# Kernel tuning notes

Measured on AMD Instinct MI355X. Metric: run time of the kernel, lower is better.

The kernel has to match this reference:

```python
import jax, jax.numpy as jnp
import numpy as np

LMAX = 5
RESOLUTION = 12
ASPECT_RATIO = 2
BATCH = 256
NB = 2 * RESOLUTION                       # res_beta = 24
NA = round(2 * ASPECT_RATIO * RESOLUTION)  # res_alpha = res_gamma = 48
DIM = sum((2 * l + 1) ** 2 for l in range(LMAX + 1))  # 286

# normalize2mom constant for tanh: (E_{z~N(0,1)}[tanh(z)^2])^{-1/2}
_x = np.linspace(-12.0, 12.0, 1_000_001)
_pdf = np.exp(-0.5 * _x * _x) / np.sqrt(2.0 * np.pi)
ACT_CST = float(np.trapz(np.tanh(_x) ** 2 * _pdf, _x) ** -0.5)  # ~1.5927


def _su2_generators(j):
    m = np.arange(-j, j)
    raising = np.diag(-np.sqrt(j * (j + 1) - m * (m + 1)), k=-1).astype(complex)
    m = np.arange(-j + 1, j + 1)
    lowering = np.diag(np.sqrt(j * (j + 1) - m * (m - 1)), k=1).astype(complex)
    m = np.arange(-j, j + 1)
    return np.stack([0.5 * (raising + lowering), np.diag(1j * m), -0.5j * (raising - lowering)])


def _q_real_to_complex(l):
    q = np.zeros((2 * l + 1, 2 * l + 1), dtype=complex)
    for m in range(-l, 0):
        q[l + m, l + abs(m)] = 1 / np.sqrt(2)
        q[l + m, l - abs(m)] = -1j / np.sqrt(2)
    q[l, l] = 1
    for m in range(1, l + 1):
        q[l + m, l + abs(m)] = (-1) ** m / np.sqrt(2)
        q[l + m, l - abs(m)] = 1j * (-1) ** m / np.sqrt(2)
    return (-1j) ** l * q


def _so3_generators(l):
    X = _su2_generators(l)
    Q = _q_real_to_complex(l)
    return np.real(np.conj(Q.T)[None] @ X @ Q[None])  # real [3, 2l+1, 2l+1]


def _expm_angles(A, t):
    """exp(t_n * A) for real antisymmetric A via eigendecomposition. -> [n, d, d] real"""
    vals, vecs = np.linalg.eig(A.astype(complex))
    inv = np.linalg.inv(vecs)
    phases = np.exp(t[:, None] * vals[None, :])  # [n, d]
    return np.real(np.einsum('ij,nj,jk->nik', vecs, phases, inv))


def _build_D_and_qw():
    # Euler angle grids (e3nn SO3Grid convention)
    b = (np.arange(NB) + 0.5) / NB * np.pi          # beta   [nb]
    a = np.arange(NA) / NA * 2.0 * np.pi            # alpha=gamma [na]
    blocks = []
    for l in range(LMAX + 1):
        X = _so3_generators(l)
        Ra = _expm_angles(X[1], a)   # exp(alpha * X1)  [na,d,d]
        Rb = _expm_angles(X[0], b)   # exp(beta  * X0)  [nb,d,d]
        # D^l(a,b,c) = Ra[a] @ Rb[b] @ Ra[c]
        Dl = np.einsum('xij,yjk,zkl->xyzil', Ra, Rb, Ra)
        blocks.append(np.sqrt(2 * l + 1) * Dl.reshape(NA, NB, NA, -1))
    D = np.concatenate(blocks, axis=-1).astype(np.float32)  # [na, nb, na, dim]
    # lie_learn / Kostelec-Rockmore quadrature weights for beta
    bb = NB // 2
    k = np.arange(bb)
    j = np.arange(2 * bb)
    w = (2.0 / bb) * np.sin(np.pi * (2 * j + 1) / (4.0 * bb)) * np.sum(
        (1.0 / (2 * k + 1))[None, :]
        * np.sin((2 * j[:, None] + 1) * (2 * k[None, :] + 1) * np.pi / (4.0 * bb)),
        axis=1,
    )
    w = w / (2.0 * (2 * bb) ** 2)
    qw = (w * NB ** 2 / NA ** 2).astype(np.float32)  # [nb]
    return jnp.asarray(D), jnp.asarray(qw)


def setup_inputs() -> dict:
    key = jax.random.key(0)
    features = jax.random.normal(key, (BATCH, DIM), dtype=jnp.float32)
    D, qw = _build_D_and_qw()
    return {"features": features, "D": D, "qw": qw}


def reference(features, D, qw):
    dim = D.shape[-1]
    s = jnp.sqrt(jnp.asarray(dim, features.dtype))
    # to_grid: [B, dim] x [na, nb, na, dim] -> [B, na, nb, na]
    g = jnp.einsum('bi,xyzi->bxyz', features, D) / s
    # normalized pointwise nonlinearity on SO(3) samples
    g = ACT_CST * jnp.tanh(g)
    # from_grid: quadrature-weighted projection back onto flat Wigner basis
    return jnp.einsum('bxyz,y,xyzi->bi', g, qw, D) * s
```

## Files before the change

### kernel.cpp

```cpp
#include <hip/hip_runtime.h>
#include <hip/hip_bf16.h>

#define DIM    286
#define DIMP   288
#define NZTOT  55296
#define NBATCH 256
#define NB_    24
#define NA_    48
#define ZC     32
#define NTILES 1728
#define NCHUNK 192
#define TILES_PER_WG 9
#define S_CONST 16.911534525287763f
#define INV_S   0.05913123959890826f
#define ACT_CST 1.5927f

typedef short bf16x8 __attribute__((ext_vector_type(8)));
typedef float f32x4  __attribute__((ext_vector_type(4)));

#define WS_FBF  0u
#define WS_DBF  147456u
#define WS_DT   (WS_DBF + 31850496u)
#define WS_PART (WS_DT + 31850496u)

typedef const __attribute__((address_space(1))) char GA;
typedef __attribute__((address_space(3))) char LA;
__device__ __forceinline__ void gload_lds16(const void* g, void* l) {
    __builtin_amdgcn_global_load_lds((GA*)g, (LA*)l, 16, 0, 0);
}

__global__ void k_prep(const float* __restrict__ F, const float* __restrict__ D,
                       const float* __restrict__ qw,
                       __hip_bfloat16* __restrict__ Fbf,
                       __hip_bfloat16* __restrict__ Dbf, __hip_bfloat16* __restrict__ Dt2) {
    __shared__ float T[32][305];
    __shared__ float qs[24];
    int t = threadIdx.x;
    int bid = blockIdx.x;
    if (bid >= NTILES) {
        int o = (bid - NTILES) * 256 + t;
        int row = o / DIMP, col = o % DIMP;
        float v = (col < DIM) ? F[row * DIM + col] * INV_S : 0.f;
        Fbf[o] = __float2bfloat16(v);
        return;
    }
    int z0 = bid * 32;
    if (t < 24) qs[t] = qw[t] * S_CONST;
    const float4* Df = (const float4*)(D + (size_t)z0 * DIM);
    for (int k = 0; k < 9; ++k) {
        int idx = t + k * 256;
        if (idx < 2288) {
            float4 v = Df[idx];
            int e = idx * 4;
            int z = e / DIM, i = e % DIM;
            __hip_bfloat162 lo, hi;
            lo.x = __float2bfloat16(v.x); lo.y = __float2bfloat16(v.y);
            hi.x = __float2bfloat16(v.z); hi.y = __float2bfloat16(v.w);
            T[z][i] = v.x; T[z][i + 1] = v.y;
            *(__hip_bfloat162*)(Dbf + (size_t)(z0 + z) * DIMP + i) = lo;
            if (i == 284) {
                T[z + 1][0] = v.z; T[z + 1][1] = v.w;
                *(__hip_bfloat162*)(Dbf + (size_t)(z0 + z + 1) * DIMP) = hi;
            } else {
                T[z][i + 2] = v.z; T[z][i + 3] = v.w;
                *(__hip_bfloat162*)(Dbf + (size_t)(z0 + z) * DIMP + i + 2) = hi;
            }
        }
    }
    if (t < 32) {
        __hip_bfloat162 zz; zz.x = __float2bfloat16(0.f); zz.y = zz.x;
        *(__hip_bfloat162*)(Dbf + (size_t)(z0 + t) * DIMP + DIM) = zz;
    }
    __syncthreads();
    for (int s = 0; s < 5; ++s) {
        int idx = t + s * 256;
        if (idx < 1152) {
            int i = idx >> 2, zc = idx & 3;
            __hip_bfloat16 o8[8];
            #pragma unroll
            for (int j = 0; j < 8; ++j) {
                int zl = zc * 8 + j;
                int y = ((z0 + zl) / NA_) % NB_;
                o8[j] = __float2bfloat16(T[zl][i] * qs[y]);
            }
            *(bf16x8*)(Dt2 + ((size_t)bid * DIMP + i) * ZC + zc * 8) = *(const bf16x8*)o8;
        }
    }
}

__launch_bounds__(256, 2)
__global__ void k_main(const __hip_bfloat16* __restrict__ Fbf,
                       const __hip_bfloat16* __restrict__ Dbf,
                       const __hip_bfloat16* __restrict__ Dt2,
                       float* __restrict__ part) {
    __shared__ __align__(16) __hip_bfloat16 Ds[2][32][288];
    __shared__ __align__(16) __hip_bfloat16 Dts[2][288][32];
    __shared__ __align__(16) __hip_bfloat16 Gs[4][16][40];

    int t = threadIdx.x;
    int wave = t >> 6, lane = t & 63, ln = lane & 15, q = lane >> 4;

    bf16x8 fa[9];
    int row = blockIdx.y * 64 + wave * 16 + ln;
    const __hip_bfloat16* fp = Fbf + (size_t)row * DIMP + q * 8;
    #pragma unroll
    for (int ks = 0; ks < 9; ++ks) fa[ks] = *(const bf16x8*)(fp + ks * 32);

    f32x4 acc[18];
    #pragma unroll
    for (int n = 0; n < 18; ++n) acc[n] = (f32x4){0.f, 0.f, 0.f, 0.f};

    auto stage = [&](int tz, int b) {
        const char* src; char* dst;
        if (wave < 2) {
            src = (const char*)(Dbf + (size_t)tz * ZC * DIMP) + wave * 9216 + lane * 16;
            dst = ((char*)&Ds[b][0][0]) + wave * 9216;
        } else {
            src = (const char*)(Dt2 + (size_t)tz * DIMP * ZC) + (wave - 2) * 9216 + lane * 16;
            dst = ((char*)&Dts[b][0][0]) + (wave - 2) * 9216;
        }
        #pragma unroll
        for (int j = 0; j < 9; ++j)
            gload_lds16(src + j * 1024, dst + j * 1024);
    };

    stage(blockIdx.x, 0);

    #pragma unroll 1
    for (int k = 0; k < TILES_PER_WG; ++k) {
        asm volatile("s_waitcnt vmcnt(0)" ::: "memory");
        __syncthreads();
        if (k + 1 < TILES_PER_WG) stage(blockIdx.x + (k + 1) * NCHUNK, (k + 1) & 1);
        int b = k & 1;
        f32x4 g0 = (f32x4){0.f,0.f,0.f,0.f}, g1 = (f32x4){0.f,0.f,0.f,0.f};
        #pragma unroll
        for (int ks = 0; ks < 9; ++ks) {
            bf16x8 b0 = *(const bf16x8*)(&Ds[b][ln][ks * 32 + q * 8]);
            bf16x8 b1 = *(const bf16x8*)(&Ds[b][16 + ln][ks * 32 + q * 8]);
            g0 = __builtin_amdgcn_mfma_f32_16x16x32_bf16(fa[ks], b0, g0, 0, 0, 0);
            g1 = __builtin_amdgcn_mfma_f32_16x16x32_bf16(fa[ks], b1, g1, 0, 0, 0);
        }
        #pragma unroll
        for (int nf = 0; nf < 2; ++nf) {
            #pragma unroll
            for (int r = 0; r < 4; ++r) {
                float x = (nf == 0) ? g0[r] : g1[r];
                float a = fabsf(x);
                float e = __expf(-2.f * a);
                float th = (1.f - e) / (1.f + e);
                float v = copysignf(ACT_CST * th, x);
                Gs[wave][q * 4 + r][nf * 16 + ln] = __float2bfloat16(v);
            }
        }
        bf16x8 a2 = *(const bf16x8*)(&Gs[wave][ln][q * 8]);
        #pragma unroll
        for (int nf = 0; nf < 18; ++nf) {
            bf16x8 b2 = *(const bf16x8*)(&Dts[b][nf * 16 + ln][q * 8]);
            acc[nf] = __builtin_amdgcn_mfma_f32_16x16x32_bf16(a2, b2, acc[nf], 0, 0, 0);
        }
    }
    float* pb = part + ((size_t)blockIdx.x * NBATCH + blockIdx.y * 64 + wave * 16) * DIMP;
    #pragma unroll
    for (int nf = 0; nf < 18; ++nf) {
        #pragma unroll
        for (int r = 0; r < 4; ++r) {
            pb[(size_t)(q * 4 + r) * DIMP + nf * 16 + ln] = acc[nf][r];
        }
    }
}

__global__ void k_reduce(const float* __restrict__ part, float* __restrict__ out) {
    __shared__ float4 red[3][16];
    int t = threadIdx.x, wave = t >> 6, lane = t & 63;
    int j = lane & 15;
    int zg = wave * 4 + (lane >> 4);
    int o4 = blockIdx.x * 16 + j;
    int b = o4 / 72, c4 = o4 % 72;
    const float* p = part + (size_t)b * DIMP + c4 * 4;
    float4 s = make_float4(0.f, 0.f, 0.f, 0.f);
    #pragma unroll 4
    for (int ii = 0; ii < 12; ++ii) {
        float4 v = *(const float4*)(p + (size_t)(zg * 12 + ii) * NBATCH * DIMP);
        s.x += v.x; s.y += v.y; s.z += v.z; s.w += v.w;
    }
    s.x += __shfl_down(s.x, 16); s.y += __shfl_down(s.y, 16);
    s.z += __shfl_down(s.z, 16); s.w += __shfl_down(s.w, 16);
    s.x += __shfl_down(s.x, 32); s.y += __shfl_down(s.y, 32);
    s.z += __shfl_down(s.z, 32); s.w += __shfl_down(s.w, 32);
    if (wave > 0 && lane < 16) red[wave - 1][lane] = s;
    __syncthreads();
    if (wave == 0 && lane < 16) {
        #pragma unroll
        for (int w = 0; w < 3; ++w) {
            float4 v = red[w][lane];
            s.x += v.x; s.y += v.y; s.z += v.z; s.w += v.w;
        }
        int i0 = c4 * 4;
        float sv[4] = {s.x, s.y, s.z, s.w};
        #pragma unroll
        for (int kk = 0; kk < 4; ++kk)
            if (i0 + kk < DIM) out[b * DIM + i0 + kk] = sv[kk];
    }
}

extern "C" void kernel_launch(void* const* d_in, const int* in_sizes, int n_in,
                              void* d_out, int out_size, void* d_ws, size_t ws_size,
                              hipStream_t stream) {
    const float* F  = (const float*)d_in[0];
    const float* D  = (const float*)d_in[1];
    const float* qw = (const float*)d_in[2];
    char* ws = (char*)d_ws;
    __hip_bfloat16* Fbf = (__hip_bfloat16*)(ws + WS_FBF);
    __hip_bfloat16* Dbf = (__hip_bfloat16*)(ws + WS_DBF);
    __hip_bfloat16* Dt2 = (__hip_bfloat16*)(ws + WS_DT);
    float* part = (float*)(ws + WS_PART);

    k_prep<<<NTILES + 288, 256, 0, stream>>>(F, D, qw, Fbf, Dbf, Dt2);
    k_main<<<dim3(NCHUNK, 4), 256, 0, stream>>>(Fbf, Dbf, Dt2, part);
    k_reduce<<<1152, 256, 0, stream>>>(part, (float*)d_out);
}
```

Before: 160.7 us.

## Single-buffer LDS in main kernel, raise occupancy, store partials in bf16

Drops the double-buffered LDS staging in k_main for a single buffer with a load-then-compute loop and an extra barrier, and raises launch bounds to 4 blocks per CU. Partial sums are written as bf16 instead of fp32, which halves partial-buffer traffic, and the reduce kernel reads 8 bf16 per lane with half the blocks. The aim is to cut memory traffic for the partials and hide latency through occupancy rather than prefetching. The cost is that load/compute overlap within a block is lost, and bf16 partial sums reduce accuracy. With 768 blocks, higher occupancy may not materialize.

```diff
diff --git a/kernel.cpp b/kernel.cpp
--- a/kernel.cpp
+++ b/kernel.cpp
@@ -88,14 +88,14 @@
     }
 }
 
-__launch_bounds__(256, 2)
+__launch_bounds__(256, 4)
 __global__ void k_main(const __hip_bfloat16* __restrict__ Fbf,
                        const __hip_bfloat16* __restrict__ Dbf,
                        const __hip_bfloat16* __restrict__ Dt2,
-                       float* __restrict__ part) {
-    __shared__ __align__(16) __hip_bfloat16 Ds[2][32][288];
-    __shared__ __align__(16) __hip_bfloat16 Dts[2][288][32];
-    __shared__ __align__(16) __hip_bfloat16 Gs[4][16][40];
+                       __hip_bfloat16* __restrict__ part) {
+    __shared__ __align__(16) __hip_bfloat16 Ds[32][288];
+    __shared__ __align__(16) __hip_bfloat16 Dts[288][32];
+    __shared__ __align__(16) __hip_bfloat16 Gs[4][16][32];
 
     int t = threadIdx.x;
     int wave = t >> 6, lane = t & 63, ln = lane & 15, q = lane >> 4;
@@ -110,33 +110,29 @@
     #pragma unroll
     for (int n = 0; n < 18; ++n) acc[n] = (f32x4){0.f, 0.f, 0.f, 0.f};
 
-    auto stage = [&](int tz, int b) {
-        const char* src; char* dst;
-        if (wave < 2) {
-            src = (const char*)(Dbf + (size_t)tz * ZC * DIMP) + wave * 9216 + lane * 16;
-            dst = ((char*)&Ds[b][0][0]) + wave * 9216;
-        } else {
-            src = (const char*)(Dt2 + (size_t)tz * DIMP * ZC) + (wave - 2) * 9216 + lane * 16;
-            dst = ((char*)&Dts[b][0][0]) + (wave - 2) * 9216;
-        }
-        #pragma unroll
-        for (int j = 0; j < 9; ++j)
-            gload_lds16(src + j * 1024, dst + j * 1024);
-    };
-
-    stage(blockIdx.x, 0);
-
     #pragma unroll 1
     for (int k = 0; k < TILES_PER_WG; ++k) {
+        int tz = blockIdx.x + k * NCHUNK;
+        {
+            const char* src; char* dst;
+            if (wave < 2) {
+                src = (const char*)(Dbf + (size_t)tz * ZC * DIMP) + wave * 9216 + lane * 16;
+                dst = ((char*)&Ds[0][0]) + wave * 9216;
+            } else {
+                src = (const char*)(Dt2 + (size_t)tz * DIMP * ZC) + (wave - 2) * 9216 + lane * 16;
+                dst = ((char*)&Dts[0][0]) + (wave - 2) * 9216;
+            }
+            #pragma unroll
+            for (int j = 0; j < 9; ++j)
+                gload_lds16(src + j * 1024, dst + j * 1024);
+        }
         asm volatile("s_waitcnt vmcnt(0)" ::: "memory");
         __syncthreads();
-        if (k + 1 < TILES_PER_WG) stage(blockIdx.x + (k + 1) * NCHUNK, (k + 1) & 1);
-        int b = k & 1;
         f32x4 g0 = (f32x4){0.f,0.f,0.f,0.f}, g1 = (f32x4){0.f,0.f,0.f,0.f};
         #pragma unroll
         for (int ks = 0; ks < 9; ++ks) {
-            bf16x8 b0 = *(const bf16x8*)(&Ds[b][ln][ks * 32 + q * 8]);
-            bf16x8 b1 = *(const bf16x8*)(&Ds[b][16 + ln][ks * 32 + q * 8]);
+            bf16x8 b0 = *(const bf16x8*)(&Ds[ln][ks * 32 + q * 8]);
+            bf16x8 b1 = *(const bf16x8*)(&Ds[16 + ln][ks * 32 + q * 8]);
             g0 = __builtin_amdgcn_mfma_f32_16x16x32_bf16(fa[ks], b0, g0, 0, 0, 0);
             g1 = __builtin_amdgcn_mfma_f32_16x16x32_bf16(fa[ks], b1, g1, 0, 0, 0);
         }
@@ -155,51 +151,60 @@
         bf16x8 a2 = *(const bf16x8*)(&Gs[wave][ln][q * 8]);
         #pragma unroll
         for (int nf = 0; nf < 18; ++nf) {
-            bf16x8 b2 = *(const bf16x8*)(&Dts[b][nf * 16 + ln][q * 8]);
+            bf16x8 b2 = *(const bf16x8*)(&Dts[nf * 16 + ln][q * 8]);
             acc[nf] = __builtin_amdgcn_mfma_f32_16x16x32_bf16(a2, b2, acc[nf], 0, 0, 0);
         }
-    }
-    float* pb = part + ((size_t)blockIdx.x * NBATCH + blockIdx.y * 64 + wave * 16) * DIMP;
+        __syncthreads();
+    }
+    __hip_bfloat16* pb = part + ((size_t)blockIdx.x * NBATCH + blockIdx.y * 64 + wave * 16) * DIMP;
     #pragma unroll
     for (int nf = 0; nf < 18; ++nf) {
         #pragma unroll
         for (int r = 0; r < 4; ++r) {
-            pb[(size_t)(q * 4 + r) * DIMP + nf * 16 + ln] = acc[nf][r];
-        }
-    }
-}
-
-__global__ void k_reduce(const float* __restrict__ part, float* __restrict__ out) {
-    __shared__ float4 red[3][16];
+            pb[(size_t)(q * 4 + r) * DIMP + nf * 16 + ln] = __float2bfloat16(acc[nf][r]);
+        }
+    }
+}
+
+__global__ void k_reduce(const __hip_bfloat16* __restrict__ part, float* __restrict__ out) {
+    __shared__ float red[3][16][8];
     int t = threadIdx.x, wave = t >> 6, lane = t & 63;
     int j = lane & 15;
     int zg = wave * 4 + (lane >> 4);
-    int o4 = blockIdx.x * 16 + j;
-    int b = o4 / 72, c4 = o4 % 72;
-    const float* p = part + (size_t)b * DIMP + c4 * 4;
-    float4 s = make_float4(0.f, 0.f, 0.f, 0.f);
+    int o8 = blockIdx.x * 16 + j;
+    int b = o8 / 36, c8 = o8 % 36;
+    const __hip_bfloat16* p = part + (size_t)b * DIMP + c8 * 8;
+    float s[8];
+    #pragma unroll
+    for (int kk = 0; kk < 8; ++kk) s[kk] = 0.f;
     #pragma unroll 4
     for (int ii = 0; ii < 12; ++ii) {
-        float4 v = *(const float4*)(p + (size_t)(zg * 12 + ii) * NBATCH * DIMP);
-        s.x += v.x; s.y += v.y; s.z += v.z; s.w += v.w;
-    }
-    s.x += __shfl_down(s.x, 16); s.y += __shfl_down(s.y, 16);
-    s.z += __shfl_down(s.z, 16); s.w += __shfl_down(s.w, 16);
-    s.x += __shfl_down(s.x, 32); s.y += __shfl_down(s.y, 32);
-    s.z += __shfl_down(s.z, 32); s.w += __shfl_down(s.w, 32);
-    if (wave > 0 && lane < 16) red[wave - 1][lane] = s;
+        bf16x8 v = *(const bf16x8*)(p + (size_t)(zg * 12 + ii) * NBATCH * DIMP);
+        #pragma unroll
+        for (int kk = 0; kk < 8; ++kk) {
+            __hip_bfloat16 h; *(short*)&h = v[kk];
+            s[kk] += __bfloat162float(h);
+        }
+    }
+    #pragma unroll
+    for (int kk = 0; kk < 8; ++kk) {
+        s[kk] += __shfl_down(s[kk], 16);
+        s[kk] += __shfl_down(s[kk], 32);
+    }
+    if (wave > 0 && lane < 16) {
+        #pragma unroll
+        for (int kk = 0; kk < 8; ++kk) red[wave - 1][lane][kk] = s[kk];
+    }
     __syncthreads();
     if (wave == 0 && lane < 16) {
         #pragma unroll
-        for (int w = 0; w < 3; ++w) {
-            float4 v = red[w][lane];
-            s.x += v.x; s.y += v.y; s.z += v.z; s.w += v.w;
-        }
-        int i0 = c4 * 4;
-        float sv[4] = {s.x, s.y, s.z, s.w};
-        #pragma unroll
-        for (int kk = 0; kk < 4; ++kk)
-            if (i0 + kk < DIM) out[b * DIM + i0 + kk] = sv[kk];
+        for (int w = 0; w < 3; ++w)
+            #pragma unroll
+            for (int kk = 0; kk < 8; ++kk) s[kk] += red[w][lane][kk];
+        int i0 = c8 * 8;
+        #pragma unroll
+        for (int kk = 0; kk < 8; ++kk)
+            if (i0 + kk < DIM) out[b * DIM + i0 + kk] = s[kk];
     }
 }
 
@@ -213,9 +218,9 @@
     __hip_bfloat16* Fbf = (__hip_bfloat16*)(ws + WS_FBF);
     __hip_bfloat16* Dbf = (__hip_bfloat16*)(ws + WS_DBF);
     __hip_bfloat16* Dt2 = (__hip_bfloat16*)(ws + WS_DT);
-    float* part = (float*)(ws + WS_PART);
+    __hip_bfloat16* part = (__hip_bfloat16*)(ws + WS_PART);
 
     k_prep<<<NTILES + 288, 256, 0, stream>>>(F, D, qw, Fbf, Dbf, Dt2);
     k_main<<<dim3(NCHUNK, 4), 256, 0, stream>>>(Fbf, Dbf, Dt2, part);
-    k_reduce<<<1152, 256, 0, stream>>>(part, (float*)d_out);
-}
+    k_reduce<<<576, 256, 0, stream>>>(part, (float*)d_out);
+}
```

Result: no change. 159.3 us (-0.9%).
